# Performance work log

Hardware: AMD Instinct MI355X
Metric: run time of the kernel (lower is better)

## Reference

```python
import jax, jax.numpy as jnp
import numpy as np

N = 50000        # nodes
E = 800000       # directed edges (before self-loops)
F_IN = 128       # input node features
HID = 32         # hidden channels per head
HEADS = 4
NCLS = 8
EPS_BN = 1e-5
NEG_SLOPE = 0.2  # GATConv LeakyReLU default


def setup_inputs() -> dict:
    key = jax.random.key(0)
    ks = jax.random.split(key, 16)
    rn = lambda k, shape, s=0.1: jax.random.normal(k, shape, jnp.float32) * s
    inp = {}
    inp["x"] = jax.random.normal(ks[0], (N, F_IN), jnp.float32)
    inp["edge_index"] = jax.random.randint(ks[1], (2, E), 0, N, dtype=jnp.int32)
    # layer 0: F_IN -> HEADS*HID (concat)
    inp["W0"] = rn(ks[2], (F_IN, HEADS * HID))
    inp["as0"] = rn(ks[3], (HEADS, HID))
    inp["ad0"] = rn(ks[4], (HEADS, HID))
    inp["b0"] = jnp.zeros((HEADS * HID,), jnp.float32)
    inp["g0"] = jnp.ones((HEADS * HID,), jnp.float32)
    inp["bb0"] = jnp.zeros((HEADS * HID,), jnp.float32)
    inp["rm0"] = jnp.zeros((HEADS * HID,), jnp.float32)
    inp["rv0"] = jnp.ones((HEADS * HID,), jnp.float32)
    # layer 1: HEADS*HID -> HEADS*HID (concat)
    inp["W1"] = rn(ks[5], (HEADS * HID, HEADS * HID))
    inp["as1"] = rn(ks[6], (HEADS, HID))
    inp["ad1"] = rn(ks[7], (HEADS, HID))
    inp["b1"] = jnp.zeros((HEADS * HID,), jnp.float32)
    inp["g1"] = jnp.ones((HEADS * HID,), jnp.float32)
    inp["bb1"] = jnp.zeros((HEADS * HID,), jnp.float32)
    inp["rm1"] = jnp.zeros((HEADS * HID,), jnp.float32)
    inp["rv1"] = jnp.ones((HEADS * HID,), jnp.float32)
    # layer 2: HEADS*HID -> NCLS, heads=1, concat=False
    inp["W2"] = rn(ks[8], (HEADS * HID, NCLS))
    inp["as2"] = rn(ks[9], (1, NCLS))
    inp["ad2"] = rn(ks[10], (1, NCLS))
    inp["b2"] = jnp.zeros((NCLS,), jnp.float32)
    return inp


def gat_conv(x, src, dst, W, att_s, att_d, bias, H, C, concat):
    """PyG-style GATConv (eval mode, self-loops already appended to src/dst)."""
    n = x.shape[0]
    h = (x @ W).reshape(n, H, C)                       # [N,H,C]
    a_s = (h * att_s).sum(-1)                          # [N,H]
    a_d = (h * att_d).sum(-1)                          # [N,H]
    e = jax.nn.leaky_relu(a_s[src] + a_d[dst], NEG_SLOPE)  # [E,H]
    # numerically-stable segment softmax over incoming edges of each dst node
    m = jax.ops.segment_max(e, dst, num_segments=n)
    m = jnp.where(jnp.isfinite(m), m, 0.0)
    ex = jnp.exp(e - m[dst])
    den = jax.ops.segment_sum(ex, dst, num_segments=n)
    alpha = ex / (den[dst] + 1e-16)                    # [E,H]
    out = jax.ops.segment_sum(h[src] * alpha[:, :, None], dst, num_segments=n)  # [N,H,C]
    out = out.reshape(n, H * C) if concat else out.mean(axis=1)
    return out + bias


def bn_eval(x, g, b, rm, rv):
    return (x - rm) * jax.lax.rsqrt(rv + EPS_BN) * g + b


def reference(x, edge_index, W0, as0, ad0, b0, g0, bb0, rm0, rv0,
              W1, as1, ad1, b1, g1, bb1, rm1, rv1, W2, as2, ad2, b2):
    n = x.shape[0]
    loop = jnp.arange(n, dtype=edge_index.dtype)       # self-loops (PyG default)
    src = jnp.concatenate([edge_index[0], loop])
    dst = jnp.concatenate([edge_index[1], loop])
    h = gat_conv(x, src, dst, W0, as0, ad0, b0, HEADS, HID, True)
    h = jax.nn.elu(bn_eval(h, g0, bb0, rm0, rv0))
    h = gat_conv(h, src, dst, W1, as1, ad1, b1, HEADS, HID, True)
    h = jax.nn.elu(bn_eval(h, g1, bb1, rm1, rv1))
    h = gat_conv(h, src, dst, W2, as2, ad2, b2, 1, NCLS, False)
    return jax.nn.log_softmax(h, axis=1)
```

## Files before the change

kernel.cpp:

```cpp
#include <hip/hip_runtime.h>
#include <math.h>

#define N_NODES 50000
#define N_EDGES 800000
#define ET (N_EDGES + N_NODES)
#define FDIM 128
#define HEADS 4
#define HID 32
#define NCLS 8
#define NEG 0.2f
#define EPS_BN 1e-5f

#define BSH 8
#define NBUCK ((N_NODES + 255) >> BSH)
#define EPB 4096

typedef __attribute__((ext_vector_type(8))) short short8;
typedef __attribute__((ext_vector_type(4))) float f32x4;

__device__ __forceinline__ float lrelu(float e) { return e > 0.f ? e : NEG * e; }
__device__ __forceinline__ float bflo(unsigned u) { return __uint_as_float(u << 16); }
__device__ __forceinline__ float bfhi(unsigned u) { return __uint_as_float(u & 0xffff0000u); }
__device__ __forceinline__ unsigned f2bf(float f) {
    unsigned b = __float_as_uint(f);
    return (b + 0x7fffu + ((b >> 16) & 1u)) >> 16;
}


__global__ __launch_bounds__(256) void bucket_hist(const int* __restrict__ ei,
                                                   int* __restrict__ bhist) {
    __shared__ unsigned h[NBUCK];
    int tid = threadIdx.x;
    int e0 = blockIdx.x * EPB;
    for (int i = tid; i < NBUCK; i += 256) h[i] = 0;
    __syncthreads();
    #pragma unroll
    for (int k = 0; k < EPB / 256; k++) {
        int e = e0 + k * 256 + tid;
        if (e < ET) {
            int d = (e < N_EDGES) ? ei[N_EDGES + e] : (e - N_EDGES);
            atomicAdd(&h[d >> BSH], 1u);
        }
    }
    __syncthreads();
    for (int i = tid; i < NBUCK; i += 256)
        if (h[i]) atomicAdd(&bhist[i], (int)h[i]);
}

__global__ __launch_bounds__(256) void scan_buckets(const int* __restrict__ bhist,
                                                    int* __restrict__ boffs,
                                                    int* __restrict__ bcur,
                                                    int* __restrict__ offs) {
    __shared__ int s[256];
    int tid = threadIdx.x;
    int v = (tid < NBUCK) ? bhist[tid] : 0;
    s[tid] = v;
    __syncthreads();
    for (int off = 1; off < 256; off <<= 1) {
        int x = (tid >= off) ? s[tid - off] : 0;
        __syncthreads();
        s[tid] += x;
        __syncthreads();
    }
    int excl = s[tid] - v;
    if (tid < NBUCK) { boffs[tid] = excl; bcur[tid] = excl; }
    if (tid == 0) { boffs[NBUCK] = ET; offs[N_NODES] = ET; }
}

__global__ __launch_bounds__(256) void partition_pairs(const int* __restrict__ ei,
                                                       int* __restrict__ bcur,
                                                       int2* __restrict__ pairs) {
    __shared__ unsigned hist[NBUCK];
    __shared__ unsigned base[NBUCK];
    int tid = threadIdx.x;
    int e0 = blockIdx.x * EPB;
    for (int i = tid; i < NBUCK; i += 256) hist[i] = 0;
    __syncthreads();
    #pragma unroll
    for (int k = 0; k < EPB / 256; k++) {
        int e = e0 + k * 256 + tid;
        if (e < ET) {
            int d = (e < N_EDGES) ? ei[N_EDGES + e] : (e - N_EDGES);
            atomicAdd(&hist[d >> BSH], 1u);
        }
    }
    __syncthreads();
    for (int i = tid; i < NBUCK; i += 256) {
        unsigned h = hist[i];
        base[i] = h ? (unsigned)atomicAdd(&bcur[i], (int)h) : 0u;
        hist[i] = 0;
    }
    __syncthreads();
    #pragma unroll
    for (int k = 0; k < EPB / 256; k++) {
        int e = e0 + k * 256 + tid;
        if (e < ET) {
            int s, d;
            if (e < N_EDGES) { s = ei[e]; d = ei[N_EDGES + e]; }
            else             { s = d = e - N_EDGES; }
            int b = d >> BSH;
            unsigned lpos = atomicAdd(&hist[b], 1u);
            pairs[base[b] + lpos] = make_int2(s, d);
        }
    }
}

__global__ __launch_bounds__(256) void group_bucket(const int2* __restrict__ pairs,
                                                    const int* __restrict__ boffs,
                                                    int* __restrict__ offs,
                                                    int* __restrict__ ssrc) {
    __shared__ int cnt[256];
    __shared__ int pfx[256];
    int b = blockIdx.x, tid = threadIdx.x;
    int n0 = b << BSH;
    int base = boffs[b], end = boffs[b + 1];
    cnt[tid] = 0;
    __syncthreads();
    for (int i = base + tid; i < end; i += 256)
        atomicAdd(&cnt[pairs[i].y & 255], 1);
    __syncthreads();
    int v = cnt[tid];
    pfx[tid] = v;
    __syncthreads();
    for (int off = 1; off < 256; off <<= 1) {
        int x = (tid >= off) ? pfx[tid - off] : 0;
        __syncthreads();
        pfx[tid] += x;
        __syncthreads();
    }
    int excl = pfx[tid] - v;
    if (n0 + tid < N_NODES) offs[n0 + tid] = base + excl;
    cnt[tid] = excl;
    __syncthreads();
    for (int i = base + tid; i < end; i += 256) {
        int2 p = pairs[i];
        int pos = atomicAdd(&cnt[p.y & 255], 1);
        ssrc[base + pos] = p.x;
    }
}


#define CAST_B 3125
#define PACK_B 64

__global__ void prep_inputs(const float* __restrict__ x, unsigned short* __restrict__ xb,
                            const float* __restrict__ W0, unsigned short* __restrict__ W0p,
                            const float* __restrict__ W1, unsigned short* __restrict__ W1p) {
    int b = blockIdx.x, tid = threadIdx.x;
    if (b < CAST_B) {
        int i = b * 256 + tid;
        const float4* p = (const float4*)x + (size_t)i * 2;
        float4 a = p[0], c = p[1];
        uint4 o;
        o.x = f2bf(a.x) | (f2bf(a.y) << 16);
        o.y = f2bf(a.z) | (f2bf(a.w) << 16);
        o.z = f2bf(c.x) | (f2bf(c.y) << 16);
        o.w = f2bf(c.z) | (f2bf(c.w) << 16);
        ((uint4*)xb)[i] = o;
    } else {
        int pb = b - CAST_B;
        const float* W = (pb < PACK_B) ? W0 : W1;
        unsigned short* Wp = (pb < PACK_B) ? W0p : W1p;
        int o = (pb & (PACK_B - 1)) * 256 + tid;
        int j = o & 7, lane = (o >> 3) & 63, kc = (o >> 9) & 3, t = o >> 11;
        int k = kc * 32 + ((lane >> 4) << 3) + j;
        int n = t * 16 + (lane & 15);
        Wp[o] = (unsigned short)f2bf(W[k * 128 + n]);
    }
}


__global__ __launch_bounds__(256) void gemm_attn(
        const unsigned short* __restrict__ Ab, const unsigned short* __restrict__ Wp,
        const float* __restrict__ att_s, const float* __restrict__ att_d,
        unsigned short* __restrict__ Hb, float* __restrict__ asn, float* __restrict__ adn,
        int M) {
    __shared__ float tiles[64 * 132];
    int tid = threadIdx.x;
    int wv = tid >> 6, lane = tid & 63;
    int base = blockIdx.x * 64;
    int mrow = base + wv * 16 + (lane & 15);
    if (mrow >= M) mrow = M - 1;
    int koff = (lane >> 4) * 8;

    f32x4 acc[8];
    #pragma unroll
    for (int t = 0; t < 8; t++) acc[t] = (f32x4){0.f, 0.f, 0.f, 0.f};

    #pragma unroll
    for (int kc = 0; kc < 4; kc++) {
        short8 a = *(const short8*)(Ab + (size_t)mrow * 128 + kc * 32 + koff);
        #pragma unroll
        for (int t = 0; t < 8; t++) {
            short8 b = *(const short8*)(Wp + (((t * 4 + kc) * 64 + lane) << 3));
            acc[t] = __builtin_amdgcn_mfma_f32_16x16x32_bf16(a, b, acc[t], 0, 0, 0);
        }
    }

    int rbase = wv * 16 + (lane >> 4) * 4;
    int col = lane & 15;
    #pragma unroll
    for (int t = 0; t < 8; t++)
        #pragma unroll
        for (int r = 0; r < 4; r++)
            tiles[(rbase + r) * 132 + t * 16 + col] = acc[t][r];
    __syncthreads();

    #pragma unroll
    for (int it = 0; it < 4; it++) {
        int u = tid + it * 256;
        int rl = u >> 4, cg = u & 15;
        int row = base + rl;
        if (row < M) {
            const float* p = tiles + rl * 132 + cg * 8;
            float4 v0 = *(const float4*)(p);
            float4 v1 = *(const float4*)(p + 4);
            uint4 o;
            o.x = f2bf(v0.x) | (f2bf(v0.y) << 16);
            o.y = f2bf(v0.z) | (f2bf(v0.w) << 16);
            o.z = f2bf(v1.x) | (f2bf(v1.y) << 16);
            o.w = f2bf(v1.z) | (f2bf(v1.w) << 16);
            *(uint4*)(Hb + (size_t)row * 128 + cg * 8) = o;
        }
    }

    {
        int rl = tid >> 2, hd = tid & 3;
        int row = base + rl;
        if (row < M) {
            const float* hrow = tiles + rl * 132 + hd * 32;
            const float* as = att_s + hd * 32;
            const float* ad = att_d + hd * 32;
            float ps = 0.f, pd = 0.f;
            #pragma unroll
            for (int i = 0; i < 8; i++) {
                float4 hv = *(const float4*)(hrow + i * 4);
                float4 sv = *(const float4*)(as + i * 4);
                float4 dv = *(const float4*)(ad + i * 4);
                ps += hv.x * sv.x + hv.y * sv.y + hv.z * sv.z + hv.w * sv.w;
                pd += hv.x * dv.x + hv.y * dv.y + hv.z * dv.z + hv.w * dv.w;
            }
            asn[row * 4 + hd] = ps;
            adn[row * 4 + hd] = pd;
        }
    }
}


__global__ __launch_bounds__(256) void aggregate(
        const unsigned short* __restrict__ hb, const float* __restrict__ asn,
        const float* __restrict__ adn, const int* __restrict__ offs,
        const int* __restrict__ ssrc, const float* __restrict__ bias,
        const float* __restrict__ gamma, const float* __restrict__ beta,
        const float* __restrict__ rmean, const float* __restrict__ rvar,
        unsigned short* __restrict__ outb) {
    __shared__ int2 sPair[4][4][72];
    int wv = threadIdx.x >> 6;
    int node = blockIdx.x * 4 + wv;
    if (node >= N_NODES) return;
    int lane = threadIdx.x & 63;
    int hd = lane >> 4;
    int beg = offs[node], deg = offs[node + 1] - beg;
    float4 ad4 = *(const float4*)(adn + node * 4);

    if (lane < 32) sPair[wv][lane >> 3][64 + (lane & 7)] = make_int2(0, 0);

    float4 den4 = make_float4(0.f, 0.f, 0.f, 0.f);
    float acc0 = 0.f, acc1 = 0.f;
    const unsigned short* hlane = hb + 2 * lane;
    const int2* pp = &sPair[wv][hd][0];

    auto phaseC = [&](int cnt) {
        int bound = (cnt + 7) & ~7;
        for (int i = 0; i < bound; i += 8) {
            int2 p0 = pp[i],     p1 = pp[i + 1], p2 = pp[i + 2], p3 = pp[i + 3];
            int2 p4 = pp[i + 4], p5 = pp[i + 5], p6 = pp[i + 6], p7 = pp[i + 7];
            unsigned u0 = *(const unsigned*)(hlane + (((unsigned)p0.x) << 7));
            unsigned u1 = *(const unsigned*)(hlane + (((unsigned)p1.x) << 7));
            unsigned u2 = *(const unsigned*)(hlane + (((unsigned)p2.x) << 7));
            unsigned u3 = *(const unsigned*)(hlane + (((unsigned)p3.x) << 7));
            unsigned u4 = *(const unsigned*)(hlane + (((unsigned)p4.x) << 7));
            unsigned u5 = *(const unsigned*)(hlane + (((unsigned)p5.x) << 7));
            unsigned u6 = *(const unsigned*)(hlane + (((unsigned)p6.x) << 7));
            unsigned u7 = *(const unsigned*)(hlane + (((unsigned)p7.x) << 7));
            acc0 += __int_as_float(p0.y) * bflo(u0); acc1 += __int_as_float(p0.y) * bfhi(u0);
            acc0 += __int_as_float(p1.y) * bflo(u1); acc1 += __int_as_float(p1.y) * bfhi(u1);
            acc0 += __int_as_float(p2.y) * bflo(u2); acc1 += __int_as_float(p2.y) * bfhi(u2);
            acc0 += __int_as_float(p3.y) * bflo(u3); acc1 += __int_as_float(p3.y) * bfhi(u3);
            acc0 += __int_as_float(p4.y) * bflo(u4); acc1 += __int_as_float(p4.y) * bfhi(u4);
            acc0 += __int_as_float(p5.y) * bflo(u5); acc1 += __int_as_float(p5.y) * bfhi(u5);
            acc0 += __int_as_float(p6.y) * bflo(u6); acc1 += __int_as_float(p6.y) * bfhi(u6);
            acc0 += __int_as_float(p7.y) * bflo(u7); acc1 += __int_as_float(p7.y) * bfhi(u7);
        }
    };

    for (int base0 = 0; base0 < deg; base0 += 64) {
        int j = base0 + lane;
        int s = 0;
        float4 w4 = make_float4(0.f, 0.f, 0.f, 0.f);
        if (j < deg) {
            s = ssrc[beg + j];
            float4 a = *(const float4*)(asn + s * 4);
            w4.x = __expf(lrelu(a.x + ad4.x));
            w4.y = __expf(lrelu(a.y + ad4.y));
            w4.z = __expf(lrelu(a.z + ad4.z));
            w4.w = __expf(lrelu(a.w + ad4.w));
            den4.x += w4.x; den4.y += w4.y; den4.z += w4.z; den4.w += w4.w;
        }
        sPair[wv][0][lane] = make_int2(s, __float_as_int(w4.x));
        sPair[wv][1][lane] = make_int2(s, __float_as_int(w4.y));
        sPair[wv][2][lane] = make_int2(s, __float_as_int(w4.z));
        sPair[wv][3][lane] = make_int2(s, __float_as_int(w4.w));
        int cnt = deg - base0; if (cnt > 64) cnt = 64;
        phaseC(cnt);
    }

    #pragma unroll
    for (int off = 32; off; off >>= 1) {
        den4.x += __shfl_xor(den4.x, off);
        den4.y += __shfl_xor(den4.y, off);
        den4.z += __shfl_xor(den4.z, off);
        den4.w += __shfl_xor(den4.w, off);
    }
    float den = (hd & 2) ? ((hd & 1) ? den4.w : den4.z)
                         : ((hd & 1) ? den4.y : den4.x);
    float inv = 1.f / (den + 1e-16f);

    int c0 = lane * 2;
    float2 bi = *(const float2*)(bias + c0);
    float2 gm = *(const float2*)(gamma + c0);
    float2 bt = *(const float2*)(beta + c0);
    float2 rm = *(const float2*)(rmean + c0);
    float2 rv = *(const float2*)(rvar + c0);
    float o0 = acc0 * inv + bi.x;
    float o1 = acc1 * inv + bi.y;
    o0 = (o0 - rm.x) * rsqrtf(rv.x + EPS_BN) * gm.x + bt.x;
    o1 = (o1 - rm.y) * rsqrtf(rv.y + EPS_BN) * gm.y + bt.y;
    o0 = (o0 > 0.f) ? o0 : expm1f(o0);
    o1 = (o1 > 0.f) ? o1 : expm1f(o1);
    *(unsigned*)(outb + (size_t)node * 128 + c0) = f2bf(o0) | (f2bf(o1) << 16);
}


__global__ __launch_bounds__(256) void gemm2_fused(
        const unsigned short* __restrict__ xb, const float* __restrict__ W2,
        const float* __restrict__ as2, const float* __restrict__ ad2,
        float* __restrict__ h2, float* __restrict__ asn, float* __restrict__ adn) {
    __shared__ float sW[128 * 8];
    __shared__ float sas[8], sad[8];
    int tid = threadIdx.x;
    for (int i = tid; i < 1024; i += 256) sW[i] = W2[i];
    if (tid < 8) { sas[tid] = as2[tid]; sad[tid] = ad2[tid]; }
    __syncthreads();
    int node = blockIdx.x * 256 + tid;
    if (node >= N_NODES) return;
    const uint4* xr = (const uint4*)(xb + (size_t)node * 128);
    float acc[8];
    #pragma unroll
    for (int c = 0; c < 8; c++) acc[c] = 0.f;
    for (int k8 = 0; k8 < 16; k8++) {
        uint4 u = xr[k8];
        float f[8] = { bflo(u.x), bfhi(u.x), bflo(u.y), bfhi(u.y),
                       bflo(u.z), bfhi(u.z), bflo(u.w), bfhi(u.w) };
        int kb = k8 * 8;
        #pragma unroll
        for (int q = 0; q < 8; q++)
            #pragma unroll
            for (int c = 0; c < 8; c++)
                acc[c] += f[q] * sW[(kb + q) * 8 + c];
    }
    float ps = 0.f, pd = 0.f;
    #pragma unroll
    for (int c = 0; c < 8; c++) {
        h2[(size_t)node * 8 + c] = acc[c];
        ps += acc[c] * sas[c];
        pd += acc[c] * sad[c];
    }
    asn[node] = ps;
    adn[node] = pd;
}


__global__ __launch_bounds__(256) void aggregate2(
        const float* __restrict__ h2, const float* __restrict__ asn,
        const float* __restrict__ adn, const int* __restrict__ offs,
        const int* __restrict__ ssrc, const float* __restrict__ b2,
        float* __restrict__ out) {
    __shared__ int2 sPair[4][64];
    int wv = threadIdx.x >> 6;
    int node = blockIdx.x * 4 + wv;
    if (node >= N_NODES) return;
    int lane = threadIdx.x & 63;
    int g = lane >> 3, c = lane & 7;
    int beg = offs[node], end = offs[node + 1];
    int deg = end - beg;
    float adv = adn[node];

    float den = 0.f, acc = 0.f;
    auto phaseC = [&](int cnt) {
        int nIt = (cnt + 15) >> 4;
        const int2* pp = &sPair[wv][0];
        for (int i = 0; i < nIt; i++) {
            int e = i * 16 + g;
            int2 p0 = pp[e];
            int2 p1 = pp[e + 8];
            acc += __int_as_float(p0.y) * h2[(((unsigned)p0.x) << 3) + c];
            acc += __int_as_float(p1.y) * h2[(((unsigned)p1.x) << 3) + c];
        }
    };

    for (int base = 0; base < deg; base += 64) {
        int j = base + lane;
        int s = 0; float w = 0.f;
        if (j < deg) {
            s = ssrc[beg + j];
            w = __expf(lrelu(asn[s] + adv));
            den += w;
        }
        sPair[wv][lane] = make_int2(s, __float_as_int(w));
        int cnt = deg - base; if (cnt > 64) cnt = 64;
        phaseC(cnt);
    }

    acc += __shfl_xor(acc, 8); acc += __shfl_xor(acc, 16); acc += __shfl_xor(acc, 32);
    #pragma unroll
    for (int off = 32; off; off >>= 1) den += __shfl_xor(den, off);

    float o = acc / (den + 1e-16f) + b2[c];
    float mx = o;
    mx = fmaxf(mx, __shfl_xor(mx, 1));
    mx = fmaxf(mx, __shfl_xor(mx, 2));
    mx = fmaxf(mx, __shfl_xor(mx, 4));
    float ex = __expf(o - mx);
    float sm = ex;
    sm += __shfl_xor(sm, 1); sm += __shfl_xor(sm, 2); sm += __shfl_xor(sm, 4);
    if (g == 0) out[(size_t)node * 8 + c] = o - mx - logf(sm);
}


extern "C" void kernel_launch(void* const* d_in, const int* in_sizes, int n_in,
                              void* d_out, int out_size, void* d_ws, size_t ws_size,
                              hipStream_t stream) {
    const float* x   = (const float*)d_in[0];
    const int*   ei  = (const int*)d_in[1];
    const float* W0  = (const float*)d_in[2];
    const float* as0 = (const float*)d_in[3];
    const float* ad0 = (const float*)d_in[4];
    const float* b0  = (const float*)d_in[5];
    const float* g0  = (const float*)d_in[6];
    const float* bb0 = (const float*)d_in[7];
    const float* rm0 = (const float*)d_in[8];
    const float* rv0 = (const float*)d_in[9];
    const float* W1  = (const float*)d_in[10];
    const float* as1 = (const float*)d_in[11];
    const float* ad1 = (const float*)d_in[12];
    const float* b1  = (const float*)d_in[13];
    const float* g1  = (const float*)d_in[14];
    const float* bb1 = (const float*)d_in[15];
    const float* rm1 = (const float*)d_in[16];
    const float* rv1 = (const float*)d_in[17];
    const float* W2  = (const float*)d_in[18];
    const float* as2 = (const float*)d_in[19];
    const float* ad2 = (const float*)d_in[20];
    const float* b2  = (const float*)d_in[21];
    float* out = (float*)d_out;

    char* w = (char*)d_ws;
    size_t off = 0;
    auto carve = [&](size_t bytes) {
        void* p = w + off;
        off += (bytes + 255) & ~(size_t)255;
        return p;
    };
    unsigned short* xb   = (unsigned short*)carve((size_t)N_NODES * 128 * 2);
    unsigned short* Hb   = (unsigned short*)carve((size_t)N_NODES * 128 * 2);
    unsigned short* Xb   = (unsigned short*)carve((size_t)N_NODES * 128 * 2);
    unsigned short* W0p  = (unsigned short*)carve(16384 * 2);
    unsigned short* W1p  = (unsigned short*)carve(16384 * 2);
    int*   offs   = (int*)carve((size_t)(N_NODES + 1) * 4);
    int*   bhist  = (int*)carve((size_t)NBUCK * 4);
    int*   boffs  = (int*)carve((size_t)(NBUCK + 1) * 4);
    int*   bcur   = (int*)carve((size_t)NBUCK * 4);
    int*   ssrc   = (int*)carve((size_t)ET * 4);
    int2*  pairs  = (int2*)carve((size_t)ET * 8);
    float* asn    = (float*)carve((size_t)N_NODES * 4 * 4);
    float* adn    = (float*)carve((size_t)N_NODES * 4 * 4);
    float* h2     = (float*)carve((size_t)N_NODES * 8 * 4);
    float* as2n   = (float*)carve((size_t)N_NODES * 4);
    float* ad2n   = (float*)carve((size_t)N_NODES * 4);
    (void)ws_size; (void)in_sizes; (void)n_in; (void)out_size;

    const int NB = (N_NODES + 255) / 256;
    const int GB = (N_NODES + 63) / 64;
    const int PB = (ET + EPB - 1) / EPB;

    hipMemsetAsync(bhist, 0, (size_t)NBUCK * 4, stream);
    bucket_hist<<<PB, 256, 0, stream>>>(ei, bhist);
    scan_buckets<<<1, 256, 0, stream>>>(bhist, boffs, bcur, offs);
    partition_pairs<<<PB, 256, 0, stream>>>(ei, bcur, pairs);
    group_bucket<<<NBUCK, 256, 0, stream>>>(pairs, boffs, offs, ssrc);

    prep_inputs<<<CAST_B + 2 * PACK_B, 256, 0, stream>>>(x, xb, W0, W0p, W1, W1p);

    gemm_attn<<<GB, 256, 0, stream>>>(xb, W0p, as0, ad0, Hb, asn, adn, N_NODES);
    aggregate<<<(N_NODES + 3) / 4, 256, 0, stream>>>(Hb, asn, adn, offs, ssrc,
                                                     b0, g0, bb0, rm0, rv0, Xb);
    gemm_attn<<<GB, 256, 0, stream>>>(Xb, W1p, as1, ad1, Hb, asn, adn, N_NODES);
    aggregate<<<(N_NODES + 3) / 4, 256, 0, stream>>>(Hb, asn, adn, offs, ssrc,
                                                     b1, g1, bb1, rm1, rv1, Xb);
    gemm2_fused<<<NB, 256, 0, stream>>>(Xb, W2, as2, ad2, h2, as2n, ad2n);
    aggregate2<<<(N_NODES + 3) / 4, 256, 0, stream>>>(h2, as2n, ad2n, offs, ssrc, b2, out);
}
```

Baseline: 287.4 us.

## Fuse CSR build kernels with input prep and first GEMM, shrink buckets

The bucket histogram is merged into the input-cast/weight-pack kernel, and the pair partitioning is merged with the layer-0 GEMM as extra blocks of one launch. The standalone scan kernel is removed: every partition block and every group block rescans the bucket histogram itself. Buckets shrink from 256 to 64 nodes, so there are more group blocks with less work each. The intent is fewer launches and serial tiny kernels, and overlap of the independent GEMM with the CSR build. The cost is redundant scans in every block, and the merged kernel's shared memory is sized by the GEMM tile.

```diff
diff --git a/kernel.cpp b/kernel.cpp
--- a/kernel.cpp
+++ b/kernel.cpp
@@ -11,8 +11,8 @@
 #define NEG 0.2f
 #define EPS_BN 1e-5f
 
-#define BSH 8
-#define NBUCK ((N_NODES + 255) >> BSH)
+#define BSH 6
+#define NBUCK ((N_NODES + 63) >> BSH)
 #define EPB 4096
 
 typedef __attribute__((ext_vector_type(8))) short short8;
@@ -26,126 +26,42 @@
     return (b + 0x7fffu + ((b >> 16) & 1u)) >> 16;
 }
 
-
-__global__ __launch_bounds__(256) void bucket_hist(const int* __restrict__ ei,
-                                                   int* __restrict__ bhist) {
-    __shared__ unsigned h[NBUCK];
-    int tid = threadIdx.x;
-    int e0 = blockIdx.x * EPB;
-    for (int i = tid; i < NBUCK; i += 256) h[i] = 0;
-    __syncthreads();
-    #pragma unroll
-    for (int k = 0; k < EPB / 256; k++) {
-        int e = e0 + k * 256 + tid;
-        if (e < ET) {
-            int d = (e < N_EDGES) ? ei[N_EDGES + e] : (e - N_EDGES);
-            atomicAdd(&h[d >> BSH], 1u);
-        }
-    }
-    __syncthreads();
-    for (int i = tid; i < NBUCK; i += 256)
-        if (h[i]) atomicAdd(&bhist[i], (int)h[i]);
-}
-
-__global__ __launch_bounds__(256) void scan_buckets(const int* __restrict__ bhist,
-                                                    int* __restrict__ boffs,
-                                                    int* __restrict__ bcur,
-                                                    int* __restrict__ offs) {
-    __shared__ int s[256];
-    int tid = threadIdx.x;
-    int v = (tid < NBUCK) ? bhist[tid] : 0;
-    s[tid] = v;
+__device__ __forceinline__ void scan_bhist(const int* __restrict__ bhist,
+                                           int* bloc, int* stmp) {
+    int t = threadIdx.x;
+    int idx = t * 4;
+    int v0 = (idx     < NBUCK) ? bhist[idx]     : 0;
+    int v1 = (idx + 1 < NBUCK) ? bhist[idx + 1] : 0;
+    int v2 = (idx + 2 < NBUCK) ? bhist[idx + 2] : 0;
+    int v3 = (idx + 3 < NBUCK) ? bhist[idx + 3] : 0;
+    int sum = v0 + v1 + v2 + v3;
+    stmp[t] = sum;
     __syncthreads();
     for (int off = 1; off < 256; off <<= 1) {
-        int x = (tid >= off) ? s[tid - off] : 0;
-        __syncthreads();
-        s[tid] += x;
-        __syncthreads();
-    }
-    int excl = s[tid] - v;
-    if (tid < NBUCK) { boffs[tid] = excl; bcur[tid] = excl; }
-    if (tid == 0) { boffs[NBUCK] = ET; offs[N_NODES] = ET; }
-}
-
-__global__ __launch_bounds__(256) void partition_pairs(const int* __restrict__ ei,
-                                                       int* __restrict__ bcur,
-                                                       int2* __restrict__ pairs) {
-    __shared__ unsigned hist[NBUCK];
-    __shared__ unsigned base[NBUCK];
-    int tid = threadIdx.x;
-    int e0 = blockIdx.x * EPB;
-    for (int i = tid; i < NBUCK; i += 256) hist[i] = 0;
-    __syncthreads();
-    #pragma unroll
-    for (int k = 0; k < EPB / 256; k++) {
-        int e = e0 + k * 256 + tid;
-        if (e < ET) {
-            int d = (e < N_EDGES) ? ei[N_EDGES + e] : (e - N_EDGES);
-            atomicAdd(&hist[d >> BSH], 1u);
-        }
-    }
-    __syncthreads();
-    for (int i = tid; i < NBUCK; i += 256) {
-        unsigned h = hist[i];
-        base[i] = h ? (unsigned)atomicAdd(&bcur[i], (int)h) : 0u;
-        hist[i] = 0;
-    }
-    __syncthreads();
-    #pragma unroll
-    for (int k = 0; k < EPB / 256; k++) {
-        int e = e0 + k * 256 + tid;
-        if (e < ET) {
-            int s, d;
-            if (e < N_EDGES) { s = ei[e]; d = ei[N_EDGES + e]; }
-            else             { s = d = e - N_EDGES; }
-            int b = d >> BSH;
-            unsigned lpos = atomicAdd(&hist[b], 1u);
-            pairs[base[b] + lpos] = make_int2(s, d);
-        }
-    }
-}
-
-__global__ __launch_bounds__(256) void group_bucket(const int2* __restrict__ pairs,
-                                                    const int* __restrict__ boffs,
-                                                    int* __restrict__ offs,
-                                                    int* __restrict__ ssrc) {
-    __shared__ int cnt[256];
-    __shared__ int pfx[256];
-    int b = blockIdx.x, tid = threadIdx.x;
-    int n0 = b << BSH;
-    int base = boffs[b], end = boffs[b + 1];
-    cnt[tid] = 0;
-    __syncthreads();
-    for (int i = base + tid; i < end; i += 256)
-        atomicAdd(&cnt[pairs[i].y & 255], 1);
-    __syncthreads();
-    int v = cnt[tid];
-    pfx[tid] = v;
-    __syncthreads();
-    for (int off = 1; off < 256; off <<= 1) {
-        int x = (tid >= off) ? pfx[tid - off] : 0;
-        __syncthreads();
-        pfx[tid] += x;
-        __syncthreads();
-    }
-    int excl = pfx[tid] - v;
-    if (n0 + tid < N_NODES) offs[n0 + tid] = base + excl;
-    cnt[tid] = excl;
-    __syncthreads();
-    for (int i = base + tid; i < end; i += 256) {
-        int2 p = pairs[i];
-        int pos = atomicAdd(&cnt[p.y & 255], 1);
-        ssrc[base + pos] = p.x;
-    }
+        int x = (t >= off) ? stmp[t - off] : 0;
+        __syncthreads();
+        stmp[t] += x;
+        __syncthreads();
+    }
+    int run = stmp[t] - sum;
+    if (idx     < NBUCK) bloc[idx]     = run; run += v0;
+    if (idx + 1 < NBUCK) bloc[idx + 1] = run; run += v1;
+    if (idx + 2 < NBUCK) bloc[idx + 2] = run; run += v2;
+    if (idx + 3 < NBUCK) bloc[idx + 3] = run;
+    __syncthreads();
 }
 
 
 #define CAST_B 3125
 #define PACK_B 64
-
-__global__ void prep_inputs(const float* __restrict__ x, unsigned short* __restrict__ xb,
-                            const float* __restrict__ W0, unsigned short* __restrict__ W0p,
-                            const float* __restrict__ W1, unsigned short* __restrict__ W1p) {
+#define PB ((ET + EPB - 1) / EPB)
+
+__global__ __launch_bounds__(256) void prep_hist(
+        const float* __restrict__ x, unsigned short* __restrict__ xb,
+        const float* __restrict__ W0, unsigned short* __restrict__ W0p,
+        const float* __restrict__ W1, unsigned short* __restrict__ W1p,
+        const int* __restrict__ ei, int* __restrict__ bhist) {
+    __shared__ unsigned h[NBUCK];
     int b = blockIdx.x, tid = threadIdx.x;
     if (b < CAST_B) {
         int i = b * 256 + tid;
@@ -157,7 +73,7 @@
         o.z = f2bf(c.x) | (f2bf(c.y) << 16);
         o.w = f2bf(c.z) | (f2bf(c.w) << 16);
         ((uint4*)xb)[i] = o;
-    } else {
+    } else if (b < CAST_B + 2 * PACK_B) {
         int pb = b - CAST_B;
         const float* W = (pb < PACK_B) ? W0 : W1;
         unsigned short* Wp = (pb < PACK_B) ? W0p : W1p;
@@ -166,19 +82,35 @@
         int k = kc * 32 + ((lane >> 4) << 3) + j;
         int n = t * 16 + (lane & 15);
         Wp[o] = (unsigned short)f2bf(W[k * 128 + n]);
-    }
-}
-
-
-__global__ __launch_bounds__(256) void gemm_attn(
+    } else {
+        int blk = b - (CAST_B + 2 * PACK_B);
+        int e0 = blk * EPB;
+        for (int i = tid; i < NBUCK; i += 256) h[i] = 0;
+        __syncthreads();
+        #pragma unroll
+        for (int k = 0; k < EPB / 256; k++) {
+            int e = e0 + k * 256 + tid;
+            if (e < ET) {
+                int d = (e < N_EDGES) ? ei[N_EDGES + e] : (e - N_EDGES);
+                atomicAdd(&h[d >> BSH], 1u);
+            }
+        }
+        __syncthreads();
+        for (int i = tid; i < NBUCK; i += 256)
+            if (h[i]) atomicAdd(&bhist[i], (int)h[i]);
+    }
+}
+
+
+__device__ __forceinline__ void gemm_attn_body(
+        float* tiles, int gb,
         const unsigned short* __restrict__ Ab, const unsigned short* __restrict__ Wp,
         const float* __restrict__ att_s, const float* __restrict__ att_d,
         unsigned short* __restrict__ Hb, float* __restrict__ asn, float* __restrict__ adn,
         int M) {
-    __shared__ float tiles[64 * 132];
     int tid = threadIdx.x;
     int wv = tid >> 6, lane = tid & 63;
-    int base = blockIdx.x * 64;
+    int base = gb * 64;
     int mrow = base + wv * 16 + (lane & 15);
     if (mrow >= M) mrow = M - 1;
     int koff = (lane >> 4) * 8;
@@ -192,8 +124,8 @@
         short8 a = *(const short8*)(Ab + (size_t)mrow * 128 + kc * 32 + koff);
         #pragma unroll
         for (int t = 0; t < 8; t++) {
-            short8 b = *(const short8*)(Wp + (((t * 4 + kc) * 64 + lane) << 3));
-            acc[t] = __builtin_amdgcn_mfma_f32_16x16x32_bf16(a, b, acc[t], 0, 0, 0);
+            short8 bfr = *(const short8*)(Wp + (((t * 4 + kc) * 64 + lane) << 3));
+            acc[t] = __builtin_amdgcn_mfma_f32_16x16x32_bf16(a, bfr, acc[t], 0, 0, 0);
         }
     }
 
@@ -244,6 +176,106 @@
             adn[row * 4 + hd] = pd;
         }
     }
+}
+
+
+__global__ __launch_bounds__(256) void part_gemm(
+        const int* __restrict__ ei, const int* __restrict__ bhist,
+        int* __restrict__ bcur, int2* __restrict__ pairs,
+        const unsigned short* __restrict__ Ab, const unsigned short* __restrict__ Wp,
+        const float* __restrict__ att_s, const float* __restrict__ att_d,
+        unsigned short* __restrict__ Hb, float* __restrict__ asn, float* __restrict__ adn,
+        int M) {
+    __shared__ float smem[64 * 132];
+    int tid = threadIdx.x;
+    if (blockIdx.x < PB) {
+        unsigned* hist = (unsigned*)smem;
+        unsigned* base = hist + NBUCK;
+        int* bloc = (int*)(base + NBUCK);
+        int* stmp = bloc + NBUCK;
+        for (int i = tid; i < NBUCK; i += 256) hist[i] = 0;
+        scan_bhist(bhist, bloc, stmp);
+        int e0 = blockIdx.x * EPB;
+        #pragma unroll
+        for (int k = 0; k < EPB / 256; k++) {
+            int e = e0 + k * 256 + tid;
+            if (e < ET) {
+                int d = (e < N_EDGES) ? ei[N_EDGES + e] : (e - N_EDGES);
+                atomicAdd(&hist[d >> BSH], 1u);
+            }
+        }
+        __syncthreads();
+        for (int i = tid; i < NBUCK; i += 256) {
+            unsigned h = hist[i];
+            base[i] = h ? (unsigned)(bloc[i] + atomicAdd(&bcur[i], (int)h)) : 0u;
+            hist[i] = 0;
+        }
+        __syncthreads();
+        #pragma unroll
+        for (int k = 0; k < EPB / 256; k++) {
+            int e = e0 + k * 256 + tid;
+            if (e < ET) {
+                int s, d;
+                if (e < N_EDGES) { s = ei[e]; d = ei[N_EDGES + e]; }
+                else             { s = d = e - N_EDGES; }
+                int bk = d >> BSH;
+                unsigned lpos = atomicAdd(&hist[bk], 1u);
+                pairs[base[bk] + lpos] = make_int2(s, d);
+            }
+        }
+    } else {
+        gemm_attn_body(smem, blockIdx.x - PB, Ab, Wp, att_s, att_d, Hb, asn, adn, M);
+    }
+}
+
+__global__ __launch_bounds__(256) void gemm_attn(
+        const unsigned short* __restrict__ Ab, const unsigned short* __restrict__ Wp,
+        const float* __restrict__ att_s, const float* __restrict__ att_d,
+        unsigned short* __restrict__ Hb, float* __restrict__ asn, float* __restrict__ adn,
+        int M) {
+    __shared__ float tiles[64 * 132];
+    gemm_attn_body(tiles, blockIdx.x, Ab, Wp, att_s, att_d, Hb, asn, adn, M);
+}
+
+
+__global__ __launch_bounds__(256) void group_bucket(const int2* __restrict__ pairs,
+                                                    const int* __restrict__ bhist,
+                                                    int* __restrict__ offs,
+                                                    int* __restrict__ ssrc) {
+    __shared__ int bloc[NBUCK];
+    __shared__ int stmp[256];
+    __shared__ int cnt[64];
+    int b = blockIdx.x, tid = threadIdx.x;
+    scan_bhist(bhist, bloc, stmp);
+    int base = bloc[b];
+    int end = (b + 1 < NBUCK) ? bloc[b + 1] : ET;
+    int n0 = b << BSH;
+    if (tid < 64) cnt[tid] = 0;
+    __syncthreads();
+    for (int i = base + tid; i < end; i += 256)
+        atomicAdd(&cnt[pairs[i].y & 63], 1);
+    __syncthreads();
+    int v = (tid < 64) ? cnt[tid] : 0;
+    stmp[tid] = v;
+    __syncthreads();
+    for (int off = 1; off < 64; off <<= 1) {
+        int x = (tid >= off) ? stmp[tid - off] : 0;
+        __syncthreads();
+        stmp[tid] += x;
+        __syncthreads();
+    }
+    int excl = stmp[tid] - v;
+    if (tid < 64) {
+        if (n0 + tid < N_NODES) offs[n0 + tid] = base + excl;
+        cnt[tid] = excl;
+    }
+    __syncthreads();
+    for (int i = base + tid; i < end; i += 256) {
+        int2 p = pairs[i];
+        int pos = atomicAdd(&cnt[p.y & 63], 1);
+        ssrc[base + pos] = p.x;
+    }
+    if (b == 0 && tid == 0) offs[N_NODES] = ET;
 }
 
 
@@ -478,9 +510,8 @@
     unsigned short* W0p  = (unsigned short*)carve(16384 * 2);
     unsigned short* W1p  = (unsigned short*)carve(16384 * 2);
     int*   offs   = (int*)carve((size_t)(N_NODES + 1) * 4);
-    int*   bhist  = (int*)carve((size_t)NBUCK * 4);
-    int*   boffs  = (int*)carve((size_t)(NBUCK + 1) * 4);
-    int*   bcur   = (int*)carve((size_t)NBUCK * 4);
+    int*   bhist  = (int*)carve((size_t)NBUCK * 2 * 4);
+    int*   bcur   = bhist + NBUCK;
     int*   ssrc   = (int*)carve((size_t)ET * 4);
     int2*  pairs  = (int2*)carve((size_t)ET * 8);
     float* asn    = (float*)carve((size_t)N_NODES * 4 * 4);
@@ -492,17 +523,13 @@
 
     const int NB = (N_NODES + 255) / 256;
     const int GB = (N_NODES + 63) / 64;
-    const int PB = (ET + EPB - 1) / EPB;
-
-    hipMemsetAsync(bhist, 0, (size_t)NBUCK * 4, stream);
-    bucket_hist<<<PB, 256, 0, stream>>>(ei, bhist);
-    scan_buckets<<<1, 256, 0, stream>>>(bhist, boffs, bcur, offs);
-    partition_pairs<<<PB, 256, 0, stream>>>(ei, bcur, pairs);
-    group_bucket<<<NBUCK, 256, 0, stream>>>(pairs, boffs, offs, ssrc);
-
-    prep_inputs<<<CAST_B + 2 * PACK_B, 256, 0, stream>>>(x, xb, W0, W0p, W1, W1p);
-
-    gemm_attn<<<GB, 256, 0, stream>>>(xb, W0p, as0, ad0, Hb, asn, adn, N_NODES);
+
+    hipMemsetAsync(bhist, 0, (size_t)NBUCK * 2 * 4, stream);
+    prep_hist<<<CAST_B + 2 * PACK_B + PB, 256, 0, stream>>>(x, xb, W0, W0p, W1, W1p, ei, bhist);
+    part_gemm<<<PB + GB, 256, 0, stream>>>(ei, bhist, bcur, pairs,
+                                           xb, W0p, as0, ad0, Hb, asn, adn, N_NODES);
+    group_bucket<<<NBUCK, 256, 0, stream>>>(pairs, bhist, offs, ssrc);
+
     aggregate<<<(N_NODES + 3) / 4, 256, 0, stream>>>(Hb, asn, adn, offs, ssrc,
                                                      b0, g0, bb0, rm0, rv0, Xb);
     gemm_attn<<<GB, 256, 0, stream>>>(Xb, W1p, as1, ad1, Hb, asn, adn, N_NODES);
```

Result: faster. 279.7 us (-2.7%).
